# Optimization experiments

Hardware: AMD Instinct MI355X
Metric: run time of the kernel (lower is better)

Reference implementation:

```python
import jax, jax.numpy as jnp
import numpy as np

B, D_IN, N, L, P, C = 512, 784, 2048, 6, 15, 10  # batch, input, width, dag layers, weight pairs, classes


def setup_inputs() -> dict:
    key = jax.random.key(0)
    ks = jax.random.split(key, 10)
    x = jax.random.normal(ks[0], (B, D_IN), jnp.float32)
    w_in = jax.random.normal(ks[1], (N, D_IN), jnp.float32) * 0.1
    b_in = jax.random.normal(ks[2], (N,), jnp.float32) * 0.1
    W = jax.random.normal(ks[3], (P, N, N), jnp.float32) * 0.1
    # binary 0/1 float masks standing in for DAG connectivity masks
    M = jax.random.bernoulli(ks[4], 0.5, (P, N, N)).astype(jnp.float32)
    b = jax.random.normal(ks[5], (L - 1, N), jnp.float32) * 0.1
    w_out1 = jax.random.normal(ks[6], (C, N), jnp.float32) * 0.1
    b_out1 = jax.random.normal(ks[7], (C,), jnp.float32) * 0.1
    w_out2 = jax.random.normal(ks[8], (C, N), jnp.float32) * 0.1
    b_out2 = jax.random.normal(ks[9], (C,), jnp.float32) * 0.1
    return {"x": x, "w_in": w_in, "b_in": b_in, "W": W, "M": M, "b": b,
            "w_out1": w_out1, "b_out1": b_out1, "w_out2": w_out2, "b_out2": b_out2}


def reference(x, w_in, b_in, W, M, b, w_out1, b_out1, w_out2, b_out2):
    # input layer
    acts = [jax.nn.relu(x @ w_in.T + b_in)]  # [B, N]
    idx = 0
    for i in range(1, L):  # DAG layer i has predecessors 0..i-1
        Wm = W[idx:idx + i] * M[idx:idx + i]          # [i, N, N] masked weights
        stacked = jnp.stack(acts)                      # [i, B, N]
        # sum over predecessors of inp @ Wm.T; bias added once per predecessor
        out = jnp.einsum('jbn,jmn->bm', stacked, Wm) + i * b[i - 1]
        acts.append(jax.nn.relu(out))
        idx += i
    return acts[-1] @ w_out1.T + b_out1 + acts[-2] @ w_out2.T + b_out2
```

## Files before the change

### kernel.cpp

```cpp
#include <hip/hip_runtime.h>

typedef __bf16 bf16;
typedef __attribute__((ext_vector_type(8))) __bf16 bf16x8;
typedef __attribute__((ext_vector_type(4))) __bf16 bf16x4;
typedef __attribute__((ext_vector_type(4))) float floatx4;

#define B_SZ 512
#define N_SZ 2048
#define DIN  784
#define DINP 800
#define ACT_LD 12288

__device__ __forceinline__ void load_lds16(const bf16* g, bf16* l) {
    __builtin_amdgcn_global_load_lds(
        (const __attribute__((address_space(1))) void*)g,
        (__attribute__((address_space(3))) void*)l, 16, 0, 0);
}

__global__ __launch_bounds__(256)
void prep_kernel(const float* __restrict__ x, const float* __restrict__ w_in,
                 bf16* __restrict__ xb, bf16* __restrict__ w_inb)
{
    int g = blockIdx.x * 256 + threadIdx.x;
    const int GPR = DINP / 4;
    const float* src; bf16* dst; int row, c;
    if (g < B_SZ * GPR) {
        row = g / GPR; c = g - row * GPR;
        src = x + (size_t)row * DIN;  dst = xb + (size_t)row * DINP;
    } else {
        int h = g - B_SZ * GPR;
        row = h / GPR; c = h - row * GPR;
        src = w_in + (size_t)row * DIN;  dst = w_inb + (size_t)row * DINP;
    }
    int k = c * 4;
    floatx4 v = (floatx4){0.f, 0.f, 0.f, 0.f};
    if (k < DIN) v = *(const floatx4*)(src + k);
    bf16x4 o;
    o[0] = (bf16)v[0]; o[1] = (bf16)v[1]; o[2] = (bf16)v[2]; o[3] = (bf16)v[3];
    *(bf16x4*)(dst + k) = o;
}

__global__ __launch_bounds__(256, 2)
void gemm_kernel(const bf16* __restrict__ A, int lda,
                 const bf16* __restrict__ Bm, int ldb,
                 float* __restrict__ partial,
                 int chunkK, int Ktot)
{
    __shared__ bf16 As[128 * 32];
    __shared__ bf16 Bs[128 * 32];

    const int t    = threadIdx.x;
    const int lane = t & 63, wave = t >> 6;
    const int wm   = (wave & 1) * 64, wn = (wave >> 1) * 64;
    const int l15  = lane & 15, quad = lane >> 4;
    const int n0   = blockIdx.x * 128, m0 = blockIdx.y * 128;
    const int s    = blockIdx.z;
    const int kb   = s * chunkK;
    const int ke   = (kb + chunkK < Ktot) ? (kb + chunkK) : Ktot;

    const int rA = wave * 16 + (lane >> 2);
    const int cA = (lane & 3) * 8;
    const bf16* pA0 = A  + (size_t)(m0 + rA) * lda + cA + kb;
    const bf16* pA1 = pA0 + (size_t)64 * lda;
    const bf16* pB0 = Bm + (size_t)(n0 + rA) * ldb + cA + kb;
    const bf16* pB1 = pB0 + (size_t)64 * ldb;
    bf16* dA0 = &As[wave * 512];  bf16* dA1 = &As[(wave + 4) * 512];
    bf16* dB0 = &Bs[wave * 512];  bf16* dB1 = &Bs[(wave + 4) * 512];

    floatx4 acc[4][4];
#pragma unroll
    for (int a = 0; a < 4; a++)
#pragma unroll
        for (int b = 0; b < 4; b++) acc[a][b] = (floatx4){0.f, 0.f, 0.f, 0.f};

    for (int k0 = kb; k0 < ke; k0 += 32) {
        __syncthreads();
        load_lds16(pA0, dA0);  load_lds16(pA1, dA1);
        load_lds16(pB0, dB0);  load_lds16(pB1, dB1);
        pA0 += 32; pA1 += 32; pB0 += 32; pB1 += 32;
        __syncthreads();

        bf16x8 af[4], bfr[4];
#pragma unroll
        for (int a = 0; a < 4; a++)
            af[a] = *(const bf16x8*)(&As[(wm + a * 16 + l15) * 32 + quad * 8]);
#pragma unroll
        for (int b = 0; b < 4; b++)
            bfr[b] = *(const bf16x8*)(&Bs[(wn + b * 16 + l15) * 32 + quad * 8]);
#pragma unroll
        for (int a = 0; a < 4; a++)
#pragma unroll
            for (int b = 0; b < 4; b++)
                acc[a][b] = __builtin_amdgcn_mfma_f32_16x16x32_bf16(af[a], bfr[b], acc[a][b], 0, 0, 0);
    }

    float* outp = partial + (size_t)s * (B_SZ * N_SZ);
#pragma unroll
    for (int a = 0; a < 4; a++)
#pragma unroll
        for (int b = 0; b < 4; b++)
#pragma unroll
            for (int r = 0; r < 4; r++) {
                int row = m0 + wm + a * 16 + quad * 4 + r;
                int col = n0 + wn + b * 16 + l15;
                outp[(size_t)row * N_SZ + col] = acc[a][b][r];
            }
}

__global__ __launch_bounds__(512, 2)
void dag_gemm_kernel(const bf16* __restrict__ A,
                     const float* __restrict__ Wl, const float* __restrict__ Ml,
                     float* __restrict__ partial,
                     int chunkK)
{
    __shared__ bf16 Bs[2][64 * 64];

    const int t    = threadIdx.x;
    const int lane = t & 63, wave = t >> 6;
    const int l15  = lane & 15, quad = lane >> 4;
    const int n0   = (blockIdx.x >> 3) * 64;
    const int z    = blockIdx.x & 7;
    const int kb   = z * chunkK;
    const int ke   = kb + chunkK;

    const int br = t >> 3, bc = (t & 7) * 8;
    const size_t wrow = (size_t)(n0 + br) << 11;
    bf16* bdst = &Bs[0][br * 64 + (bc ^ ((br & 7) << 3))];

    const bf16* Abase = A + (size_t)(wave * 64 + l15) * ACT_LD + quad * 8;

    floatx4 acc[4][4];
#pragma unroll
    for (int a = 0; a < 4; a++)
#pragma unroll
        for (int b = 0; b < 4; b++) acc[a][b] = (floatx4){0.f, 0.f, 0.f, 0.f};

    floatx4 w0a, w1a, m0a, m1a;
    floatx4 w0b, w1b, m0b, m1b;

#define LOAD_WM(k, w0, w1, m0, m1) do {                          \
        int jj = (k) >> 11, kk2 = (k) & 2047;                     \
        size_t o = ((size_t)jj << 22) + wrow + kk2 + bc;          \
        w0 = *(const floatx4*)(Wl + o);                           \
        w1 = *(const floatx4*)(Wl + o + 4);                       \
        m0 = *(const floatx4*)(Ml + o);                           \
        m1 = *(const floatx4*)(Ml + o + 4);                       \
    } while (0)

#define PACK(buf, w0, w1, m0, m1) do {                           \
        bf16x8 o8;                                                \
        o8[0] = (bf16)(w0[0] * m0[0]); o8[1] = (bf16)(w0[1] * m0[1]); \
        o8[2] = (bf16)(w0[2] * m0[2]); o8[3] = (bf16)(w0[3] * m0[3]); \
        o8[4] = (bf16)(w1[0] * m1[0]); o8[5] = (bf16)(w1[1] * m1[1]); \
        o8[6] = (bf16)(w1[2] * m1[2]); o8[7] = (bf16)(w1[3] * m1[3]); \
        *(bf16x8*)(bdst + (buf) * 4096) = o8;                     \
    } while (0)

    auto compute = [&](int buf, int k0) {
        bf16x8 af[8];
        const bf16* ap = Abase + k0;
#pragma unroll
        for (int a = 0; a < 4; a++) {
            af[a]     = *(const bf16x8*)(ap + (size_t)(a * 16) * ACT_LD);
            af[4 + a] = *(const bf16x8*)(ap + (size_t)(a * 16) * ACT_LD + 32);
        }
#pragma unroll
        for (int kk = 0; kk < 2; kk++) {
            bf16x8 bfr[4];
#pragma unroll
            for (int b = 0; b < 4; b++) {
                int r = b * 16 + l15;
                int e = (kk * 32 + quad * 8) ^ ((r & 7) << 3);
                bfr[b] = *(const bf16x8*)(&Bs[buf][r * 64 + e]);
            }
#pragma unroll
            for (int a = 0; a < 4; a++)
#pragma unroll
                for (int b = 0; b < 4; b++)
                    acc[a][b] = __builtin_amdgcn_mfma_f32_16x16x32_bf16(
                        af[kk * 4 + a], bfr[b], acc[a][b], 0, 0, 0);
        }
    };

    LOAD_WM(kb,       w0a, w1a, m0a, m1a);
    LOAD_WM(kb + 64,  w0b, w1b, m0b, m1b);
    PACK(0, w0a, w1a, m0a, m1a);
    LOAD_WM(kb + 128, w0a, w1a, m0a, m1a);
    __syncthreads();

    const int nt = chunkK >> 6;
    for (int tt = 0; tt < nt; tt += 2) {
        const int k0 = kb + tt * 64;
        compute(0, k0);
        PACK(1, w0b, w1b, m0b, m1b);
        if (k0 + 192 < ke) LOAD_WM(k0 + 192, w0b, w1b, m0b, m1b);
        __syncthreads();
        compute(1, k0 + 64);
        PACK(0, w0a, w1a, m0a, m1a);
        if (k0 + 256 < ke) LOAD_WM(k0 + 256, w0a, w1a, m0a, m1a);
        __syncthreads();
    }
#undef LOAD_WM
#undef PACK

    float* outp = partial + (size_t)z * (B_SZ * N_SZ);
#pragma unroll
    for (int a = 0; a < 4; a++)
#pragma unroll
        for (int b = 0; b < 4; b++)
#pragma unroll
            for (int r = 0; r < 4; r++) {
                int row = wave * 64 + a * 16 + quad * 4 + r;
                int col = n0 + b * 16 + l15;
                outp[(size_t)row * N_SZ + col] = acc[a][b][r];
            }
}

__global__ __launch_bounds__(256)
void epilogue_kernel(const float* __restrict__ partial, int S,
                     const float* __restrict__ bias, float bscale,
                     bf16* __restrict__ actdst)
{
    int g = blockIdx.x * 256 + threadIdx.x;
    size_t off = (size_t)g * 4;
    int b = (int)(off >> 11);
    int n = (int)(off & (N_SZ - 1));
    floatx4 v = *(const floatx4*)(partial + off);
    for (int s2 = 1; s2 < S; s2++)
        v += *(const floatx4*)(partial + (size_t)s2 * (B_SZ * N_SZ) + off);
    floatx4 bv = *(const floatx4*)(bias + n);
    bf16x4 o;
#pragma unroll
    for (int j = 0; j < 4; j++) {
        float xv = v[j] + bscale * bv[j];
        xv = xv > 0.f ? xv : 0.f;
        o[j] = (bf16)xv;
    }
    *(bf16x4*)(actdst + (size_t)b * ACT_LD + n) = o;
}

__global__ __launch_bounds__(64)
void out_kernel(const bf16* __restrict__ act4, const bf16* __restrict__ act5,
                const float* __restrict__ w1, const float* __restrict__ b1,
                const float* __restrict__ w2, const float* __restrict__ b2,
                float* __restrict__ out)
{
    int b = blockIdx.x, lane = threadIdx.x;
    float a5[32], a4[32];
#pragma unroll
    for (int rep = 0; rep < 4; rep++) {
        bf16x8 v5 = *(const bf16x8*)(act5 + (size_t)b * ACT_LD + rep * 512 + lane * 8);
        bf16x8 v4 = *(const bf16x8*)(act4 + (size_t)b * ACT_LD + rep * 512 + lane * 8);
#pragma unroll
        for (int j = 0; j < 8; j++) {
            a5[rep * 8 + j] = (float)v5[j];
            a4[rep * 8 + j] = (float)v4[j];
        }
    }
    for (int c = 0; c < 10; c++) {
        float d = 0.f;
#pragma unroll
        for (int rep = 0; rep < 4; rep++) {
            floatx4 wa = *(const floatx4*)(w1 + (size_t)c * N_SZ + rep * 512 + lane * 8);
            floatx4 wb = *(const floatx4*)(w1 + (size_t)c * N_SZ + rep * 512 + lane * 8 + 4);
            floatx4 va = *(const floatx4*)(w2 + (size_t)c * N_SZ + rep * 512 + lane * 8);
            floatx4 vb = *(const floatx4*)(w2 + (size_t)c * N_SZ + rep * 512 + lane * 8 + 4);
#pragma unroll
            for (int j = 0; j < 4; j++) {
                d += a5[rep * 8 + j] * wa[j] + a4[rep * 8 + j] * va[j];
                d += a5[rep * 8 + 4 + j] * wb[j] + a4[rep * 8 + 4 + j] * vb[j];
            }
        }
        for (int off = 32; off > 0; off >>= 1) d += __shfl_down(d, off);
        if (lane == 0) out[b * 10 + c] = d + b1[c] + b2[c];
    }
}

extern "C" void kernel_launch(void* const* d_in, const int* in_sizes, int n_in,
                              void* d_out, int out_size, void* d_ws, size_t ws_size,
                              hipStream_t stream)
{
    const float* x    = (const float*)d_in[0];
    const float* w_in = (const float*)d_in[1];
    const float* b_in = (const float*)d_in[2];
    const float* W    = (const float*)d_in[3];
    const float* M    = (const float*)d_in[4];
    const float* bL   = (const float*)d_in[5];
    const float* w1   = (const float*)d_in[6];
    const float* b1   = (const float*)d_in[7];
    const float* w2   = (const float*)d_in[8];
    const float* b2   = (const float*)d_in[9];
    float* out = (float*)d_out;

    char* ws = (char*)d_ws;
    bf16*  xb      = (bf16*)ws;
    bf16*  w_inb   = (bf16*)(ws + 819200);
    bf16*  actsT   = (bf16*)(ws + 4096000);
    float* partial = (float*)(ws + 16678912);

    prep_kernel<<<2000, 256, 0, stream>>>(x, w_in, xb, w_inb);

    gemm_kernel<<<dim3(16, 4, 4), 256, 0, stream>>>(
        xb, DINP, w_inb, DINP, partial, 224, DINP);
    epilogue_kernel<<<1024, 256, 0, stream>>>(partial, 4, b_in, 1.0f, actsT);

    for (int i = 1; i < 6; i++) {
        int idx = i * (i - 1) / 2;
        const float* Wl = W + ((size_t)idx << 22);
        const float* Ml = M + ((size_t)idx << 22);
        dag_gemm_kernel<<<256, 512, 0, stream>>>(
            actsT, Wl, Ml, partial, 256 * i);
        epilogue_kernel<<<1024, 256, 0, stream>>>(
            partial, 8, bL + (size_t)(i - 1) * N_SZ, (float)i,
            actsT + (size_t)i * N_SZ);
    }

    out_kernel<<<512, 64, 0, stream>>>(
        actsT + (size_t)4 * N_SZ, actsT + (size_t)5 * N_SZ,
        w1, b1, w2, b2, out);
}
```

Before: 661.8 us.

## Pre-pack masked weights to tiled swizzled bf16 and prefetch activations

A new kernel multiplies W by M, converts the product to bf16, and writes it once in a tile-contiguous, pre-swizzled layout. Each DAG GEMM block then loads its 64x64 weight tile with one coalesced 16-byte load per thread, replacing the four fp32 loads and the multiply-convert in the main loop. The loop also double-buffers activation fragments in registers so A loads overlap the MFMA work. Total memory traffic rises because of the extra bf16 write and re-read, and the change needs a larger workspace. The bet is that the GEMM was limited by latency rather than bandwidth.

```diff
diff --git a/kernel.cpp b/kernel.cpp
--- a/kernel.cpp
+++ b/kernel.cpp
@@ -40,6 +40,35 @@
     *(bf16x4*)(dst + k) = o;
 }
 
+__global__ __launch_bounds__(256)
+void wm_pack_kernel(const float* __restrict__ W, const float* __restrict__ M,
+                    bf16* __restrict__ WMb)
+{
+    size_t g = (size_t)blockIdx.x * 256 + threadIdx.x;
+    size_t e = g << 3;
+    int jj   = (int)(e >> 22);
+    int rem  = (int)(e & 4194303);
+    int r    = rem >> 11;
+    int c    = rem & 2047;
+    int ktile = c >> 6;
+    int sg    = (c >> 3) & 7;
+    int r6    = r & 63;
+    int ntile = r >> 6;
+    int ss    = sg ^ (r6 & 7);
+    size_t op = ((((size_t)jj * 32 + ntile) * 32 + ktile) << 12)
+              + ((size_t)r6 << 6) + ((size_t)ss << 3);
+    floatx4 w0 = *(const floatx4*)(W + e);
+    floatx4 w1 = *(const floatx4*)(W + e + 4);
+    floatx4 m0 = *(const floatx4*)(M + e);
+    floatx4 m1 = *(const floatx4*)(M + e + 4);
+    bf16x8 o;
+    o[0] = (bf16)(w0[0] * m0[0]); o[1] = (bf16)(w0[1] * m0[1]);
+    o[2] = (bf16)(w0[2] * m0[2]); o[3] = (bf16)(w0[3] * m0[3]);
+    o[4] = (bf16)(w1[0] * m1[0]); o[5] = (bf16)(w1[1] * m1[1]);
+    o[6] = (bf16)(w1[2] * m1[2]); o[7] = (bf16)(w1[3] * m1[3]);
+    *(bf16x8*)(WMb + op) = o;
+}
+
 __global__ __launch_bounds__(256, 2)
 void gemm_kernel(const bf16* __restrict__ A, int lda,
                  const bf16* __restrict__ Bm, int ldb,
@@ -109,25 +138,22 @@
 
 __global__ __launch_bounds__(512, 2)
 void dag_gemm_kernel(const bf16* __restrict__ A,
-                     const float* __restrict__ Wl, const float* __restrict__ Ml,
+                     const bf16* __restrict__ WMb,
                      float* __restrict__ partial,
                      int chunkK)
 {
-    __shared__ bf16 Bs[2][64 * 64];
+    __shared__ bf16 Bs[2][4096];
 
     const int t    = threadIdx.x;
     const int lane = t & 63, wave = t >> 6;
     const int l15  = lane & 15, quad = lane >> 4;
-    const int n0   = (blockIdx.x >> 3) * 64;
+    const int ntile = blockIdx.x >> 3;
     const int z    = blockIdx.x & 7;
     const int kb   = z * chunkK;
-    const int ke   = kb + chunkK;
-
-    const int br = t >> 3, bc = (t & 7) * 8;
-    const size_t wrow = (size_t)(n0 + br) << 11;
-    bf16* bdst = &Bs[0][br * 64 + (bc ^ ((br & 7) << 3))];
-
-    const bf16* Abase = A + (size_t)(wave * 64 + l15) * ACT_LD + quad * 8;
+    const int nt   = chunkK >> 6;
+    const int tile0 = kb >> 6;
+
+    const bf16* Abase = A + (size_t)(wave * 64 + l15) * ACT_LD + quad * 8 + kb;
 
     floatx4 acc[4][4];
 #pragma unroll
@@ -135,44 +161,34 @@
 #pragma unroll
         for (int b = 0; b < 4; b++) acc[a][b] = (floatx4){0.f, 0.f, 0.f, 0.f};
 
-    floatx4 w0a, w1a, m0a, m1a;
-    floatx4 w0b, w1b, m0b, m1b;
-
-#define LOAD_WM(k, w0, w1, m0, m1) do {                          \
-        int jj = (k) >> 11, kk2 = (k) & 2047;                     \
-        size_t o = ((size_t)jj << 22) + wrow + kk2 + bc;          \
-        w0 = *(const floatx4*)(Wl + o);                           \
-        w1 = *(const floatx4*)(Wl + o + 4);                       \
-        m0 = *(const floatx4*)(Ml + o);                           \
-        m1 = *(const floatx4*)(Ml + o + 4);                       \
-    } while (0)
-
-#define PACK(buf, w0, w1, m0, m1) do {                           \
-        bf16x8 o8;                                                \
-        o8[0] = (bf16)(w0[0] * m0[0]); o8[1] = (bf16)(w0[1] * m0[1]); \
-        o8[2] = (bf16)(w0[2] * m0[2]); o8[3] = (bf16)(w0[3] * m0[3]); \
-        o8[4] = (bf16)(w1[0] * m1[0]); o8[5] = (bf16)(w1[1] * m1[1]); \
-        o8[6] = (bf16)(w1[2] * m1[2]); o8[7] = (bf16)(w1[3] * m1[3]); \
-        *(bf16x8*)(bdst + (buf) * 4096) = o8;                     \
-    } while (0)
-
-    auto compute = [&](int buf, int k0) {
-        bf16x8 af[8];
-        const bf16* ap = Abase + k0;
+    bf16x8 ga, gb;
+    bf16x8 af0[8], af1[8];
+
+    auto loadWM = [&](bf16x8& g, int tt) {
+        int gt = tile0 + tt;
+        size_t off = ((((size_t)(gt >> 5) * 32 + ntile) * 32 + (gt & 31)) << 12)
+                   + ((size_t)t << 3);
+        g = *(const bf16x8*)(WMb + off);
+    };
+    auto loadA = [&](bf16x8* af, int tt) {
+        const bf16* ap = Abase + tt * 64;
 #pragma unroll
         for (int a = 0; a < 4; a++) {
             af[a]     = *(const bf16x8*)(ap + (size_t)(a * 16) * ACT_LD);
             af[4 + a] = *(const bf16x8*)(ap + (size_t)(a * 16) * ACT_LD + 32);
         }
+    };
+    auto commit = [&](int buf, const bf16x8& g) {
+        *(bf16x8*)(&Bs[buf][t << 3]) = g;
+    };
+    auto mma = [&](int buf, const bf16x8* af) {
 #pragma unroll
         for (int kk = 0; kk < 2; kk++) {
+            const int e = (kk * 32 + quad * 8) ^ ((l15 & 7) << 3);
             bf16x8 bfr[4];
 #pragma unroll
-            for (int b = 0; b < 4; b++) {
-                int r = b * 16 + l15;
-                int e = (kk * 32 + quad * 8) ^ ((r & 7) << 3);
-                bfr[b] = *(const bf16x8*)(&Bs[buf][r * 64 + e]);
-            }
+            for (int b = 0; b < 4; b++)
+                bfr[b] = *(const bf16x8*)(&Bs[buf][(b * 16 + l15) * 64 + e]);
 #pragma unroll
             for (int a = 0; a < 4; a++)
 #pragma unroll
@@ -182,26 +198,26 @@
         }
     };
 
-    LOAD_WM(kb,       w0a, w1a, m0a, m1a);
-    LOAD_WM(kb + 64,  w0b, w1b, m0b, m1b);
-    PACK(0, w0a, w1a, m0a, m1a);
-    LOAD_WM(kb + 128, w0a, w1a, m0a, m1a);
+    loadWM(ga, 0);
+    loadWM(gb, 1);
+    loadA(af0, 0);
+    commit(0, ga);
+    loadWM(ga, 2);
+    loadA(af1, 1);
     __syncthreads();
 
-    const int nt = chunkK >> 6;
     for (int tt = 0; tt < nt; tt += 2) {
-        const int k0 = kb + tt * 64;
-        compute(0, k0);
-        PACK(1, w0b, w1b, m0b, m1b);
-        if (k0 + 192 < ke) LOAD_WM(k0 + 192, w0b, w1b, m0b, m1b);
+        commit(1, gb);
+        if (tt + 3 < nt) loadWM(gb, tt + 3);
+        mma(0, af0);
+        if (tt + 2 < nt) loadA(af0, tt + 2);
         __syncthreads();
-        compute(1, k0 + 64);
-        PACK(0, w0a, w1a, m0a, m1a);
-        if (k0 + 256 < ke) LOAD_WM(k0 + 256, w0a, w1a, m0a, m1a);
+        if (tt + 2 < nt) commit(0, ga);
+        if (tt + 4 < nt) loadWM(ga, tt + 4);
+        mma(1, af1);
+        if (tt + 3 < nt) loadA(af1, tt + 3);
         __syncthreads();
     }
-#undef LOAD_WM
-#undef PACK
 
     float* outp = partial + (size_t)z * (B_SZ * N_SZ);
 #pragma unroll
@@ -211,7 +227,7 @@
 #pragma unroll
             for (int r = 0; r < 4; r++) {
                 int row = wave * 64 + a * 16 + quad * 4 + r;
-                int col = n0 + b * 16 + l15;
+                int col = ntile * 64 + b * 16 + l15;
                 outp[(size_t)row * N_SZ + col] = acc[a][b][r];
             }
 }
@@ -297,8 +313,11 @@
     bf16*  w_inb   = (bf16*)(ws + 819200);
     bf16*  actsT   = (bf16*)(ws + 4096000);
     float* partial = (float*)(ws + 16678912);
+    bf16*  WMb     = (bf16*)(ws + 50233344);
 
     prep_kernel<<<2000, 256, 0, stream>>>(x, w_in, xb, w_inb);
+
+    wm_pack_kernel<<<30720, 256, 0, stream>>>(W, M, WMb);
 
     gemm_kernel<<<dim3(16, 4, 4), 256, 0, stream>>>(
         xb, DINP, w_inb, DINP, partial, 224, DINP);
@@ -306,10 +325,9 @@
 
     for (int i = 1; i < 6; i++) {
         int idx = i * (i - 1) / 2;
-        const float* Wl = W + ((size_t)idx << 22);
-        const float* Ml = M + ((size_t)idx << 22);
+        const bf16* WMl = WMb + ((size_t)idx << 22);
         dag_gemm_kernel<<<256, 512, 0, stream>>>(
-            actsT, Wl, Ml, partial, 256 * i);
+            actsT, WMl, partial, 256 * i);
         epilogue_kernel<<<1024, 256, 0, stream>>>(
             partial, 8, bL + (size_t)(i - 1) * N_SZ, (float)i,
             actsT + (size_t)i * N_SZ);
```

After: 741.9 us. 1.12x slower.

## Software-pipeline A fragment loads and reorder LDS commit before MFMA in DAG GEMM

Applied to the files above, without the earlier changes.

Restructures the DAG GEMM main loop so the activation (A) fragments for the next tile are prefetched into registers while the current tile's MFMAs run, using two register fragment sets. The masked weight pack into LDS now happens before the MFMA block rather than after it. The full __syncthreads is replaced with an lgkmcnt wait plus s_barrier, which does not wait for outstanding global loads. The aim is to hide global load latency for A and the W/M prefetch behind matrix work, at the cost of more VGPRs under the 512-thread, 2-block launch bound.

```diff
diff --git a/kernel.cpp b/kernel.cpp
--- a/kernel.cpp
+++ b/kernel.cpp
@@ -113,7 +113,7 @@
                      float* __restrict__ partial,
                      int chunkK)
 {
-    __shared__ bf16 Bs[2][64 * 64];
+    __shared__ bf16 Bs[2][4096];
 
     const int t    = threadIdx.x;
     const int lane = t & 63, wave = t >> 6;
@@ -121,13 +121,13 @@
     const int n0   = (blockIdx.x >> 3) * 64;
     const int z    = blockIdx.x & 7;
     const int kb   = z * chunkK;
-    const int ke   = kb + chunkK;
+    const int nt   = chunkK >> 6;
 
     const int br = t >> 3, bc = (t & 7) * 8;
     const size_t wrow = (size_t)(n0 + br) << 11;
     bf16* bdst = &Bs[0][br * 64 + (bc ^ ((br & 7) << 3))];
 
-    const bf16* Abase = A + (size_t)(wave * 64 + l15) * ACT_LD + quad * 8;
+    const bf16* Abase = A + (size_t)(wave * 64 + l15) * ACT_LD + quad * 8 + kb;
 
     floatx4 acc[4][4];
 #pragma unroll
@@ -137,9 +137,11 @@
 
     floatx4 w0a, w1a, m0a, m1a;
     floatx4 w0b, w1b, m0b, m1b;
-
-#define LOAD_WM(k, w0, w1, m0, m1) do {                          \
-        int jj = (k) >> 11, kk2 = (k) & 2047;                     \
+    bf16x8 af0[8], af1[8];
+
+#define LOAD_WM(tt, w0, w1, m0, m1) do {                          \
+        int k = kb + (tt) * 64;                                   \
+        int jj = k >> 11, kk2 = k & 2047;                         \
         size_t o = ((size_t)jj << 22) + wrow + kk2 + bc;          \
         w0 = *(const floatx4*)(Wl + o);                           \
         w1 = *(const floatx4*)(Wl + o + 4);                       \
@@ -147,7 +149,7 @@
         m1 = *(const floatx4*)(Ml + o + 4);                       \
     } while (0)
 
-#define PACK(buf, w0, w1, m0, m1) do {                           \
+#define COMMIT(buf, w0, w1, m0, m1) do {                          \
         bf16x8 o8;                                                \
         o8[0] = (bf16)(w0[0] * m0[0]); o8[1] = (bf16)(w0[1] * m0[1]); \
         o8[2] = (bf16)(w0[2] * m0[2]); o8[3] = (bf16)(w0[3] * m0[3]); \
@@ -156,23 +158,27 @@
         *(bf16x8*)(bdst + (buf) * 4096) = o8;                     \
     } while (0)
 
-    auto compute = [&](int buf, int k0) {
-        bf16x8 af[8];
-        const bf16* ap = Abase + k0;
+#define BAR() do {                                                \
+        asm volatile("s_waitcnt lgkmcnt(0)" ::: "memory");        \
+        __builtin_amdgcn_s_barrier();                             \
+    } while (0)
+
+    auto loadA = [&](bf16x8* af, int tt) {
+        const bf16* ap = Abase + tt * 64;
 #pragma unroll
         for (int a = 0; a < 4; a++) {
             af[a]     = *(const bf16x8*)(ap + (size_t)(a * 16) * ACT_LD);
             af[4 + a] = *(const bf16x8*)(ap + (size_t)(a * 16) * ACT_LD + 32);
         }
+    };
+    auto mma = [&](int buf, const bf16x8* af) {
 #pragma unroll
         for (int kk = 0; kk < 2; kk++) {
+            const int e = (kk * 32 + quad * 8) ^ ((l15 & 7) << 3);
             bf16x8 bfr[4];
 #pragma unroll
-            for (int b = 0; b < 4; b++) {
-                int r = b * 16 + l15;
-                int e = (kk * 32 + quad * 8) ^ ((r & 7) << 3);
-                bfr[b] = *(const bf16x8*)(&Bs[buf][r * 64 + e]);
-            }
+            for (int b = 0; b < 4; b++)
+                bfr[b] = *(const bf16x8*)(&Bs[buf][(b * 16 + l15) * 64 + e]);
 #pragma unroll
             for (int a = 0; a < 4; a++)
 #pragma unroll
@@ -182,26 +188,29 @@
         }
     };
 
-    LOAD_WM(kb,       w0a, w1a, m0a, m1a);
-    LOAD_WM(kb + 64,  w0b, w1b, m0b, m1b);
-    PACK(0, w0a, w1a, m0a, m1a);
-    LOAD_WM(kb + 128, w0a, w1a, m0a, m1a);
-    __syncthreads();
-
-    const int nt = chunkK >> 6;
+    LOAD_WM(0, w0a, w1a, m0a, m1a);
+    LOAD_WM(1, w0b, w1b, m0b, m1b);
+    loadA(af0, 0);
+    COMMIT(0, w0a, w1a, m0a, m1a);
+    LOAD_WM(2, w0a, w1a, m0a, m1a);
+    loadA(af1, 1);
+    BAR();
+
     for (int tt = 0; tt < nt; tt += 2) {
-        const int k0 = kb + tt * 64;
-        compute(0, k0);
-        PACK(1, w0b, w1b, m0b, m1b);
-        if (k0 + 192 < ke) LOAD_WM(k0 + 192, w0b, w1b, m0b, m1b);
-        __syncthreads();
-        compute(1, k0 + 64);
-        PACK(0, w0a, w1a, m0a, m1a);
-        if (k0 + 256 < ke) LOAD_WM(k0 + 256, w0a, w1a, m0a, m1a);
-        __syncthreads();
+        COMMIT(1, w0b, w1b, m0b, m1b);
+        if (tt + 3 < nt) LOAD_WM(tt + 3, w0b, w1b, m0b, m1b);
+        mma(0, af0);
+        if (tt + 2 < nt) loadA(af0, tt + 2);
+        BAR();
+        if (tt + 2 < nt) COMMIT(0, w0a, w1a, m0a, m1a);
+        if (tt + 4 < nt) LOAD_WM(tt + 4, w0a, w1a, m0a, m1a);
+        mma(1, af1);
+        if (tt + 3 < nt) loadA(af1, tt + 3);
+        BAR();
     }
 #undef LOAD_WM
-#undef PACK
+#undef COMMIT
+#undef BAR
 
     float* outp = partial + (size_t)z * (B_SZ * N_SZ);
 #pragma unroll
```

Measured after the change: 641.7 us. 3.0% less time.
